# Performance work log

Measured on AMD Instinct MI355X. Metric: run time of the kernel, lower is better.

Reference implementation:

```python
import jax, jax.numpy as jnp
import numpy as np

A = 64    # number of discrete actions (expert matrices)
D = 512   # input/output feature dim
B = 2048  # batch size


def setup_inputs() -> dict:
    key = jax.random.key(0)
    kx, ka, kw, kb = jax.random.split(key, 4)
    stdv = 1.0 / np.sqrt(D)  # matches torch init: uniform(-stdv, stdv), stdv = 1/sqrt(weight.size(1))
    x = jax.random.normal(kx, (B, D), dtype=jnp.float32)
    a = jax.random.randint(ka, (B,), 0, A, dtype=jnp.int64)
    weight = jax.random.uniform(kw, (A, D, D), dtype=jnp.float32, minval=-stdv, maxval=stdv)
    bias = jax.random.uniform(kb, (A, D), dtype=jnp.float32, minval=-stdv, maxval=stdv)
    return {"x": x, "a": a, "weight": weight, "bias": bias}


def reference(x, a, weight, bias):
    # Per-sample weight gather + batched matvec:
    #   z[b, i] = sum_j weight[a[b], i, j] * x[b, j] + bias[a[b], i]
    w = weight[a]                              # [B, D, D] gathered per-sample matrices
    z = jnp.einsum('bij,bj->bi', w, x)         # batched matvec
    z = z + bias[a]                            # per-sample bias gather + add
    return z
```

## Files before the change

### kernel.cpp

```cpp
#include <hip/hip_runtime.h>


#define NA 64
#define DD 512
#define NB 2048
#define BN 128
#define NW 8
#define BK 32
#define NSTEPS 16
#define NSLOT 5

typedef __bf16  bf16x8  __attribute__((ext_vector_type(8)));
typedef __bf16  bf16x4  __attribute__((ext_vector_type(4)));
typedef float   floatx4 __attribute__((ext_vector_type(4)));

#define GLD16(g, l)                                                         \
  __builtin_amdgcn_global_load_lds(                                         \
      (const __attribute__((address_space(1))) void*)(g),                   \
      (__attribute__((address_space(3))) void*)(l), 16, 0, 0)
#define VMCNT(n) asm volatile("s_waitcnt vmcnt(" #n ")" ::: "memory")
#define LGKMCNT0 asm volatile("s_waitcnt lgkmcnt(0)" ::: "memory")
#define SBAR     __builtin_amdgcn_s_barrier()
#define SCHED0   __builtin_amdgcn_sched_barrier(0)

static __device__ inline bf16x8 cvt8(floatx4 lo, floatx4 hi) {
    bf16x8 r;
    r[0] = (__bf16)lo[0]; r[1] = (__bf16)lo[1];
    r[2] = (__bf16)lo[2]; r[3] = (__bf16)lo[3];
    r[4] = (__bf16)hi[0]; r[5] = (__bf16)hi[1];
    r[6] = (__bf16)hi[2]; r[7] = (__bf16)hi[3];
    return r;
}

__global__ __launch_bounds__(512, 1) void dl_fused(
        const float* __restrict__ x,
        const int*   __restrict__ act,
        const float* __restrict__ weight,
        const float* __restrict__ bias,
        float*       __restrict__ out)
{
    const int a    = blockIdx.x;
    const int tid  = threadIdx.x;
    const int wave = tid >> 6;
    const int lane = tid & 63;
    const int l16  = lane & 15;
    const int kgrp = lane >> 4;
    const int colbase = blockIdx.y * BN;
    const int ncol    = colbase + wave * 16 + l16;

    __shared__ int s_perm[NB];
    __shared__ int s_wcnt[NW];
    __shared__ __align__(16) __bf16 Xs[64][DD];
    __shared__ __align__(16) float  Wl[NSLOT][BN][BK];

    const int ibase = wave * (NB / NW);
    int myact[NB / NW / 64];
    int wcnt = 0;
#pragma unroll
    for (int it = 0; it < NB / NW / 64; ++it) {
        myact[it] = act[ibase + it * 64 + lane];
        unsigned long long m = __ballot(myact[it] == a);
        wcnt += (int)__popcll(m);
    }
    if (lane == 0) s_wcnt[wave] = wcnt;
    __syncthreads();
    int cnt = 0, off = 0;
#pragma unroll
    for (int v = 0; v < NW; ++v) {
        const int c = s_wcnt[v];
        if (v < wave) off += c;
        cnt += c;
    }
    if (cnt == 0) return;
#pragma unroll
    for (int it = 0; it < NB / NW / 64; ++it) {
        unsigned long long m = __ballot(myact[it] == a);
        if (myact[it] == a) {
            int pos = off + (int)__popcll(m & ((1ull << lane) - 1ull));
            s_perm[pos] = ibase + it * 64 + lane;
        }
        off += (int)__popcll(m);
    }
    __syncthreads();

    const float  bias_v = bias[(size_t)a * DD + ncol];
    const float* wtile  = weight + (size_t)a * DD * DD + (size_t)colbase * DD;

    const int r8 = lane >> 3;
    const int su = ((lane & 7) ^ r8) << 2;
    const int srow = tid >> 5;
    const int skk  = (tid & 31) << 2;

    for (int m0 = 0; m0 < cnt; m0 += 64) {
        const int rem    = min(cnt - m0, 64);
        const int nchunk = (rem + 15) >> 4;

        floatx4 xv[16];
#pragma unroll
        for (int i = 0; i < 4; ++i) {
            const int r  = srow + 16 * i;
            const int rr = (r < rem) ? r : (rem - 1);
            const float* xr = x + (size_t)s_perm[m0 + rr] * DD;
#pragma unroll
            for (int j = 0; j < 4; ++j)
                xv[i * 4 + j] = *(const floatx4*)(xr + skk + 128 * j);
        }

#pragma unroll
        for (int s = 0; s < 4; ++s) {
#pragma unroll
            for (int c = 0; c < 2; ++c)
                GLD16(wtile + (size_t)(wave * 16 + c * 8 + r8) * DD + s * BK + su,
                      (char*)(&Wl[s][wave * 16 + c * 8][0]));
        }

#pragma unroll
        for (int i = 0; i < 4; ++i) {
            const int r = srow + 16 * i;
            if (r < rem) {
                const int rs = (r & 7) << 3;
#pragma unroll
                for (int j = 0; j < 4; ++j) {
                    const int f0 = skk + 128 * j;
                    bf16x4 bv;
#pragma unroll
                    for (int q = 0; q < 4; ++q) bv[q] = (__bf16)xv[i * 4 + j][q];
                    *(bf16x4*)&Xs[r][f0 ^ rs] = bv;
                }
            }
        }
        LGKMCNT0; SBAR;

        floatx4 acc[4] = {{0,0,0,0},{0,0,0,0},{0,0,0,0},{0,0,0,0}};
        const int h = l16 & 7;
        const int wrow = wave * 16 + l16;

        auto compute = [&](int slot, int s) {
            const float* wl = &Wl[slot][0][0];
            const floatx4 blo = *(const floatx4*)(wl + wrow * BK + (((2 * kgrp)     ^ h) << 2));
            const floatx4 bhi = *(const floatx4*)(wl + wrow * BK + (((2 * kgrp + 1) ^ h) << 2));
            const bf16x8 bfrag = cvt8(blo, bhi);
            const int kb = (s * 32 + kgrp * 8) ^ (h << 3);
#pragma unroll
            for (int mc = 0; mc < 4; ++mc) {
                if (mc < nchunk) {
                    const bf16x8 afrag = *(const bf16x8*)&Xs[mc * 16 + l16][kb];
                    acc[mc] = __builtin_amdgcn_mfma_f32_16x16x32_bf16(
                                  afrag, bfrag, acc[mc], 0, 0, 0);
                }
            }
        };

#pragma unroll
        for (int i = 0; i < NSTEPS - 4; ++i) {
            VMCNT(6); SCHED0;
            const int s    = i + 4;
            const int slot = s % NSLOT;
#pragma unroll
            for (int c = 0; c < 2; ++c)
                GLD16(wtile + (size_t)(wave * 16 + c * 8 + r8) * DD + s * BK + su,
                      (char*)(&Wl[slot][wave * 16 + c * 8][0]));
            compute(i % NSLOT, i);
        }
        VMCNT(6); SCHED0; compute((NSTEPS - 4) % NSLOT, NSTEPS - 4);
        VMCNT(4); SCHED0; compute((NSTEPS - 3) % NSLOT, NSTEPS - 3);
        VMCNT(2); SCHED0; compute((NSTEPS - 2) % NSLOT, NSTEPS - 2);
        VMCNT(0); SCHED0; compute((NSTEPS - 1) % NSLOT, NSTEPS - 1);

#pragma unroll
        for (int mc = 0; mc < 4; ++mc) {
            if (mc < nchunk) {
#pragma unroll
                for (int r = 0; r < 4; ++r) {
                    const int mloc = mc * 16 + kgrp * 4 + r;
                    if (mloc < rem)
                        out[(size_t)s_perm[m0 + mloc] * DD + ncol] =
                            acc[mc][r] + bias_v;
                }
            }
        }
        __syncthreads();
    }
}

extern "C" void kernel_launch(void* const* d_in, const int* in_sizes, int n_in,
                              void* d_out, int out_size, void* d_ws, size_t ws_size,
                              hipStream_t stream) {
    const float* x      = (const float*)d_in[0];
    const int*   act    = (const int*)  d_in[1];
    const float* weight = (const float*)d_in[2];
    const float* bias   = (const float*)d_in[3];
    float*       out    = (float*)d_out;

    dl_fused<<<dim3(NA, DD / BN), 512, 0, stream>>>(x, act, weight, bias, out);
}
```

Before: 19.31 us.

## Prefetch weight tiles before activation scan and use double-buffered 64-wide K steps

Weight tile loads for the first two K steps are now issued right after loading the action indices, so they overlap the ballot/prefix-sum routing phase. The K loop changes from 16 steps of 32 with a 5-slot ring to 8 steps of 64 with two buffers, using a new XOR swizzle. Some __syncthreads are replaced by explicit lgkmcnt waits plus barriers. Fewer buffers in flight shrink the prefetch depth, and each wave relies on reading only its own rows of the weight buffer without a barrier.

Result: no change. 19.42 us (+0.6%).

```diff
diff --git a/kernel.cpp b/kernel.cpp
--- a/kernel.cpp
+++ b/kernel.cpp
@@ -6,9 +6,8 @@
 #define NB 2048
 #define BN 128
 #define NW 8
-#define BK 32
-#define NSTEPS 16
-#define NSLOT 5
+#define BK 64
+#define NSTEPS 8
 
 typedef __bf16  bf16x8  __attribute__((ext_vector_type(8)));
 typedef __bf16  bf16x4  __attribute__((ext_vector_type(4)));
@@ -51,19 +50,40 @@
     __shared__ int s_perm[NB];
     __shared__ int s_wcnt[NW];
     __shared__ __align__(16) __bf16 Xs[64][DD];
-    __shared__ __align__(16) float  Wl[NSLOT][BN][BK];
+    __shared__ __align__(16) float  Wl[2][BN][BK];
+
+    const float* wtile = weight + (size_t)a * DD * DD + (size_t)colbase * DD;
+
+    const int rr4 = lane >> 4;
+    const int u16 = lane & 15;
+
+    auto issue_step = [&](int slot, int s) {
+#pragma unroll
+        for (int c = 0; c < 4; ++c) {
+            const int riw = c * 4 + rr4;
+            GLD16(wtile + (size_t)(wave * 16 + riw) * DD + s * BK
+                        + ((u16 ^ riw) << 2),
+                  (char*)&Wl[slot][wave * 16 + c * 4][0]);
+        }
+    };
 
     const int ibase = wave * (NB / NW);
     int myact[NB / NW / 64];
+#pragma unroll
+    for (int it = 0; it < NB / NW / 64; ++it)
+        myact[it] = act[ibase + it * 64 + lane];
+
+    issue_step(0, 0);
+    issue_step(1, 1);
+
     int wcnt = 0;
 #pragma unroll
     for (int it = 0; it < NB / NW / 64; ++it) {
-        myact[it] = act[ibase + it * 64 + lane];
         unsigned long long m = __ballot(myact[it] == a);
         wcnt += (int)__popcll(m);
     }
     if (lane == 0) s_wcnt[wave] = wcnt;
-    __syncthreads();
+    LGKMCNT0; SBAR;
     int cnt = 0, off = 0;
 #pragma unroll
     for (int v = 0; v < NW; ++v) {
@@ -71,7 +91,7 @@
         if (v < wave) off += c;
         cnt += c;
     }
-    if (cnt == 0) return;
+    if (cnt == 0) { VMCNT(0); return; }
 #pragma unroll
     for (int it = 0; it < NB / NW / 64; ++it) {
         unsigned long long m = __ballot(myact[it] == a);
@@ -81,17 +101,15 @@
         }
         off += (int)__popcll(m);
     }
-    __syncthreads();
-
-    const float  bias_v = bias[(size_t)a * DD + ncol];
-    const float* wtile  = weight + (size_t)a * DD * DD + (size_t)colbase * DD;
-
-    const int r8 = lane >> 3;
-    const int su = ((lane & 7) ^ r8) << 2;
-    const int srow = tid >> 5;
-    const int skk  = (tid & 31) << 2;
+    LGKMCNT0; SBAR;
+
+    const float bias_v = bias[(size_t)a * DD + ncol];
+    const int   h      = l16 & 7;
+    const int   srow   = tid >> 5;
+    const int   skk    = (tid & 31) << 2;
 
     for (int m0 = 0; m0 < cnt; m0 += 64) {
+        if (m0 > 0) { issue_step(0, 0); issue_step(1, 1); }
         const int rem    = min(cnt - m0, 64);
         const int nchunk = (rem + 15) >> 4;
 
@@ -107,14 +125,6 @@
         }
 
 #pragma unroll
-        for (int s = 0; s < 4; ++s) {
-#pragma unroll
-            for (int c = 0; c < 2; ++c)
-                GLD16(wtile + (size_t)(wave * 16 + c * 8 + r8) * DD + s * BK + su,
-                      (char*)(&Wl[s][wave * 16 + c * 8][0]));
-        }
-
-#pragma unroll
         for (int i = 0; i < 4; ++i) {
             const int r = srow + 16 * i;
             if (r < rem) {
@@ -132,40 +142,36 @@
         LGKMCNT0; SBAR;
 
         floatx4 acc[4] = {{0,0,0,0},{0,0,0,0},{0,0,0,0},{0,0,0,0}};
-        const int h = l16 & 7;
-        const int wrow = wave * 16 + l16;
+        const char* wlrow0 = (const char*)&Wl[0][wave * 16 + l16][0];
+        const char* wlrow1 = (const char*)&Wl[1][wave * 16 + l16][0];
 
         auto compute = [&](int slot, int s) {
-            const float* wl = &Wl[slot][0][0];
-            const floatx4 blo = *(const floatx4*)(wl + wrow * BK + (((2 * kgrp)     ^ h) << 2));
-            const floatx4 bhi = *(const floatx4*)(wl + wrow * BK + (((2 * kgrp + 1) ^ h) << 2));
-            const bf16x8 bfrag = cvt8(blo, bhi);
-            const int kb = (s * 32 + kgrp * 8) ^ (h << 3);
-#pragma unroll
-            for (int mc = 0; mc < 4; ++mc) {
-                if (mc < nchunk) {
-                    const bf16x8 afrag = *(const bf16x8*)&Xs[mc * 16 + l16][kb];
-                    acc[mc] = __builtin_amdgcn_mfma_f32_16x16x32_bf16(
-                                  afrag, bfrag, acc[mc], 0, 0, 0);
+            const char* wl = slot ? wlrow1 : wlrow0;
+#pragma unroll
+            for (int s2 = 0; s2 < 2; ++s2) {
+                const int u0 = s2 * 8 + kgrp * 2;
+                const floatx4 blo = *(const floatx4*)(wl + (((u0)     ^ l16) << 4));
+                const floatx4 bhi = *(const floatx4*)(wl + (((u0 + 1) ^ l16) << 4));
+                const bf16x8 bfrag = cvt8(blo, bhi);
+                const int kb = (s * BK + s2 * 32 + kgrp * 8) ^ (h << 3);
+#pragma unroll
+                for (int mc = 0; mc < 4; ++mc) {
+                    if (mc < nchunk) {
+                        const bf16x8 afrag = *(const bf16x8*)&Xs[mc * 16 + l16][kb];
+                        acc[mc] = __builtin_amdgcn_mfma_f32_16x16x32_bf16(
+                                      afrag, bfrag, acc[mc], 0, 0, 0);
+                    }
                 }
             }
         };
 
 #pragma unroll
-        for (int i = 0; i < NSTEPS - 4; ++i) {
-            VMCNT(6); SCHED0;
-            const int s    = i + 4;
-            const int slot = s % NSLOT;
-#pragma unroll
-            for (int c = 0; c < 2; ++c)
-                GLD16(wtile + (size_t)(wave * 16 + c * 8 + r8) * DD + s * BK + su,
-                      (char*)(&Wl[slot][wave * 16 + c * 8][0]));
-            compute(i % NSLOT, i);
-        }
-        VMCNT(6); SCHED0; compute((NSTEPS - 4) % NSLOT, NSTEPS - 4);
-        VMCNT(4); SCHED0; compute((NSTEPS - 3) % NSLOT, NSTEPS - 3);
-        VMCNT(2); SCHED0; compute((NSTEPS - 2) % NSLOT, NSTEPS - 2);
-        VMCNT(0); SCHED0; compute((NSTEPS - 1) % NSLOT, NSTEPS - 1);
+        for (int i = 0; i < NSTEPS; ++i) {
+            if (i < NSTEPS - 1) { VMCNT(4); } else { VMCNT(0); }
+            SCHED0;
+            compute(i & 1, i);
+            if (i + 2 < NSTEPS) issue_step(i & 1, i + 2);
+        }
 
 #pragma unroll
         for (int mc = 0; mc < 4; ++mc) {
@@ -179,7 +185,7 @@
                 }
             }
         }
-        __syncthreads();
+        LGKMCNT0; SBAR;
     }
 }
 
```
